# Kernel tuning notes

Hardware: AMD Instinct MI355X
Metric: run time of the kernel (lower is better)

## Reference

```python
import jax, jax.numpy as jnp
import numpy as np

NUM_FEATURES = 8
HIDDEN_DIM = 256
NUM_STABILIZERS = 2048
B, S = 128, 2048


def setup_inputs() -> dict:
    key = jax.random.key(0)
    ks = jax.random.split(key, 8)
    x = jax.random.normal(ks[0], (B, S, NUM_FEATURES), dtype=jnp.float32)
    final_mask = jax.random.randint(ks[1], (B, S), 0, 3, dtype=jnp.int64)
    # stacked per-feature Linear(1, hidden): W[f, h] = weight of proj f, b[f, h] = bias
    xav = float(np.sqrt(6.0 / (1 + HIDDEN_DIM)))  # xavier_uniform for Linear(1, H)
    W = jax.random.uniform(ks[2], (NUM_FEATURES, HIDDEN_DIM), minval=-xav, maxval=xav, dtype=jnp.float32)
    b = jnp.zeros((NUM_FEATURES, HIDDEN_DIM), dtype=jnp.float32)
    index_embed = 0.02 * jax.random.normal(ks[3], (NUM_STABILIZERS, HIDDEN_DIM), dtype=jnp.float32)
    final_on = jax.random.normal(ks[4], (HIDDEN_DIM,), dtype=jnp.float32)
    final_off = jax.random.normal(ks[5], (HIDDEN_DIM,), dtype=jnp.float32)
    gamma = jnp.ones((HIDDEN_DIM,), dtype=jnp.float32)
    beta = jnp.zeros((HIDDEN_DIM,), dtype=jnp.float32)
    return {"x": x, "final_mask": final_mask, "W": W, "b": b,
            "index_embed": index_embed, "final_on": final_on,
            "final_off": final_off, "gamma": gamma, "beta": beta}


def reference(x, final_mask, W, b, index_embed, final_on, final_off, gamma, beta):
    Bx, Sx, _ = x.shape
    # sum of per-feature Linear(1,H): single GEMM + summed bias
    h = jnp.einsum('bsf,fh->bsh', x, W) + b.sum(axis=0)  # [B,S,H]
    h = h + index_embed[:Sx][None, :, :]
    h = h + (final_mask == 1)[..., None] * final_on
    h = h + (final_mask == 2)[..., None] * final_off
    # LayerNorm over last dim, eps=1e-5 (torch default)
    mu = h.mean(axis=-1, keepdims=True)
    var = h.var(axis=-1, keepdims=True)
    h = (h - mu) * jax.lax.rsqrt(var + 1e-5)
    return h * gamma + beta
```

## Files before the change

kernel.cpp:

```cpp
#include <hip/hip_runtime.h>

#define HID 256
#define NFEAT 8
#define SLEN 2048

__global__ __launch_bounds__(256) void p0_base_kernel(
    const float* __restrict__ bias,
    const float* __restrict__ ie,
    float* __restrict__ base2,
    int total4)
{
    const int idx = blockIdx.x * blockDim.x + threadIdx.x;
    if (idx >= total4) return;
    const int h0 = (idx & (HID / 4 - 1)) << 2;
    float4 r = *reinterpret_cast<const float4*>(ie + (size_t)idx * 4);
#pragma unroll
    for (int f = 0; f < NFEAT; ++f) {
        const float4 b4 = *reinterpret_cast<const float4*>(bias + f * HID + h0);
        r.x += b4.x; r.y += b4.y; r.z += b4.z; r.w += b4.w;
    }
    *reinterpret_cast<float4*>(base2 + (size_t)idx * 4) = r;
}

__global__ __launch_bounds__(256, 4) void a_stats_kernel(
    const float* __restrict__ x,
    const int*   __restrict__ mask,
    const float* __restrict__ W,
    const float* __restrict__ base2,
    const float* __restrict__ fon,
    const float* __restrict__ foff,
    float2* __restrict__ musig,
    int Bdim, int ntokens)
{
    const int lane  = threadIdx.x & 63;
    const int gwave = (blockIdx.x * blockDim.x + threadIdx.x) >> 6;
    const int s     = gwave >> 1;
    const int b     = ((gwave & 1) << 6) + lane;
    if (b >= Bdim) return;
    const int t = b * SLEN + s;

    const float4 x0 = *reinterpret_cast<const float4*>(x + (size_t)t * NFEAT);
    const float4 x1 = *reinterpret_cast<const float4*>(x + (size_t)t * NFEAT + 4);
    const float xs[NFEAT] = {x0.x, x0.y, x0.z, x0.w, x1.x, x1.y, x1.z, x1.w};
    const int m = mask[t];
    const float fm1 = (m == 1) ? 1.0f : 0.0f;
    const float fm2 = (m == 2) ? 1.0f : 0.0f;

    float s1 = 0.0f, s2 = 0.0f;
    for (int h0 = 0; h0 < HID; h0 += 4) {
        float4 acc = *reinterpret_cast<const float4*>(base2 + s * HID + h0);
#pragma unroll
        for (int f = 0; f < NFEAT; ++f) {
            const float4 w4 = *reinterpret_cast<const float4*>(W + f * HID + h0);
            acc.x = fmaf(xs[f], w4.x, acc.x);
            acc.y = fmaf(xs[f], w4.y, acc.y);
            acc.z = fmaf(xs[f], w4.z, acc.z);
            acc.w = fmaf(xs[f], w4.w, acc.w);
        }
        const float4 on4 = *reinterpret_cast<const float4*>(fon  + h0);
        const float4 of4 = *reinterpret_cast<const float4*>(foff + h0);
        acc.x += fm1 * on4.x + fm2 * of4.x;
        acc.y += fm1 * on4.y + fm2 * of4.y;
        acc.z += fm1 * on4.z + fm2 * of4.z;
        acc.w += fm1 * on4.w + fm2 * of4.w;
        s1 += acc.x + acc.y + acc.z + acc.w;
        s2 = fmaf(acc.x, acc.x, s2);
        s2 = fmaf(acc.y, acc.y, s2);
        s2 = fmaf(acc.z, acc.z, s2);
        s2 = fmaf(acc.w, acc.w, s2);
    }
    const float mu   = s1 * (1.0f / HID);
    const float var  = s2 * (1.0f / HID) - mu * mu;
    const float rstd = rsqrtf(var + 1e-5f);
    musig[t] = make_float2(mu, rstd);
}

__global__ __launch_bounds__(256, 4) void b_apply_kernel(
    const float* __restrict__ x,
    const int*   __restrict__ mask,
    const float* __restrict__ W,
    const float* __restrict__ base2,
    const float* __restrict__ fon,
    const float* __restrict__ foff,
    const float* __restrict__ gamma,
    const float* __restrict__ beta,
    const float2* __restrict__ musig,
    float* __restrict__ out,
    int ntokens)
{
    const int lane = threadIdx.x & 63;
    const int wavesPerBlock = blockDim.x >> 6;
    const int gwave = blockIdx.x * wavesPerBlock + (threadIdx.x >> 6);
    const int nwaves = gridDim.x * wavesPerBlock;
    const int h0 = lane << 2;

    float wc[NFEAT][4];
#pragma unroll
    for (int f = 0; f < NFEAT; ++f) {
        const float4 w4 = *reinterpret_cast<const float4*>(W + f * HID + h0);
        wc[f][0] = w4.x; wc[f][1] = w4.y; wc[f][2] = w4.z; wc[f][3] = w4.w;
    }
    const float4 g4  = *reinterpret_cast<const float4*>(gamma + h0);
    const float4 be4 = *reinterpret_cast<const float4*>(beta  + h0);

    for (int t = gwave; t < ntokens; t += nwaves) {
        const int s = t & (SLEN - 1);

        const float2 ms = musig[t];
        float4 acc = *reinterpret_cast<const float4*>(base2 + (size_t)s * HID + h0);
        const float4 x0 = *reinterpret_cast<const float4*>(x + (size_t)t * NFEAT);
        const float4 x1 = *reinterpret_cast<const float4*>(x + (size_t)t * NFEAT + 4);
        const int m = mask[t];

        if (m == 1) {
            const float4 on4 = *reinterpret_cast<const float4*>(fon + h0);
            acc.x += on4.x; acc.y += on4.y; acc.z += on4.z; acc.w += on4.w;
        } else if (m == 2) {
            const float4 of4 = *reinterpret_cast<const float4*>(foff + h0);
            acc.x += of4.x; acc.y += of4.y; acc.z += of4.z; acc.w += of4.w;
        }

        const float xs[NFEAT] = {x0.x, x0.y, x0.z, x0.w, x1.x, x1.y, x1.z, x1.w};
#pragma unroll
        for (int f = 0; f < NFEAT; ++f) {
            acc.x = fmaf(xs[f], wc[f][0], acc.x);
            acc.y = fmaf(xs[f], wc[f][1], acc.y);
            acc.z = fmaf(xs[f], wc[f][2], acc.z);
            acc.w = fmaf(xs[f], wc[f][3], acc.w);
        }

        float4 o4;
        o4.x = (acc.x - ms.x) * ms.y * g4.x + be4.x;
        o4.y = (acc.y - ms.x) * ms.y * g4.y + be4.y;
        o4.z = (acc.z - ms.x) * ms.y * g4.z + be4.z;
        o4.w = (acc.w - ms.x) * ms.y * g4.w + be4.w;
        *reinterpret_cast<float4*>(out + (size_t)t * HID + h0) = o4;
    }
}

extern "C" void kernel_launch(void* const* d_in, const int* in_sizes, int n_in,
                              void* d_out, int out_size, void* d_ws, size_t ws_size,
                              hipStream_t stream) {
    const float* x     = (const float*)d_in[0];
    const int*   mask  = (const int*)  d_in[1];
    const float* W     = (const float*)d_in[2];
    const float* bias  = (const float*)d_in[3];
    const float* ie    = (const float*)d_in[4];
    const float* fon   = (const float*)d_in[5];
    const float* foff  = (const float*)d_in[6];
    const float* gamma = (const float*)d_in[7];
    const float* beta  = (const float*)d_in[8];
    float* out = (float*)d_out;

    const int ntokens = in_sizes[0] / NFEAT;
    const int Bdim    = ntokens / SLEN;

    float*  base2 = (float*)d_ws;
    float2* musig = (float2*)((char*)d_ws + (size_t)SLEN * HID * sizeof(float));

    {
        const int total4 = SLEN * HID / 4;
        p0_base_kernel<<<(total4 + 255) / 256, 256, 0, stream>>>(bias, ie, base2, total4);
    }
    {
        const int waves = 2 * SLEN;
        a_stats_kernel<<<(waves * 64) / 256, 256, 0, stream>>>(
            x, mask, W, base2, fon, foff, musig, Bdim, ntokens);
    }
    {
        b_apply_kernel<<<2048, 256, 0, stream>>>(
            x, mask, W, base2, fon, foff, gamma, beta, musig, out, ntokens);
    }
}
```

Measured before the change: 327.7 us.

## Compute LayerNorm stats algebraically from precomputed Gram tables instead of per-hidden loop

Row mean and variance are now computed in closed form: a build kernel precomputes per-position dot products of the base vector with W, on and off, plus a W Gram matrix and related constants. The stats kernel then evaluates a small quadratic form over the 8 features, replacing the 256-wide loop it ran per token. The apply kernel also hoists the on/off loads, unrolls its token loop by two, and writes output with nontemporal stores. The expanded variance formula can lose precision through cancellation.

```diff
diff --git a/kernel.cpp b/kernel.cpp
--- a/kernel.cpp
+++ b/kernel.cpp
@@ -4,38 +4,100 @@
 #define NFEAT 8
 #define SLEN 2048
 
-__global__ __launch_bounds__(256) void p0_base_kernel(
-    const float* __restrict__ bias,
-    const float* __restrict__ ie,
-    float* __restrict__ base2,
-    int total4)
+typedef float v4f __attribute__((ext_vector_type(4)));
+
+__device__ __forceinline__ float wave_sum(float v) {
+#pragma unroll
+    for (int o = 32; o > 0; o >>= 1) v += __shfl_xor(v, o, 64);
+    return v;
+}
+
+__global__ __launch_bounds__(64) void k1_build(
+    const float* __restrict__ bias, const float* __restrict__ ie,
+    const float* __restrict__ W,    const float* __restrict__ fon,
+    const float* __restrict__ foff,
+    float* __restrict__ base2, float* __restrict__ tab, float* __restrict__ cst)
 {
-    const int idx = blockIdx.x * blockDim.x + threadIdx.x;
-    if (idx >= total4) return;
-    const int h0 = (idx & (HID / 4 - 1)) << 2;
-    float4 r = *reinterpret_cast<const float4*>(ie + (size_t)idx * 4);
+    const int lane = threadIdx.x;
+    const int h0 = lane << 2;
+
+    float wc[NFEAT][4];
 #pragma unroll
     for (int f = 0; f < NFEAT; ++f) {
-        const float4 b4 = *reinterpret_cast<const float4*>(bias + f * HID + h0);
-        r.x += b4.x; r.y += b4.y; r.z += b4.z; r.w += b4.w;
-    }
-    *reinterpret_cast<float4*>(base2 + (size_t)idx * 4) = r;
-}
-
-__global__ __launch_bounds__(256, 4) void a_stats_kernel(
-    const float* __restrict__ x,
-    const int*   __restrict__ mask,
-    const float* __restrict__ W,
-    const float* __restrict__ base2,
-    const float* __restrict__ fon,
-    const float* __restrict__ foff,
-    float2* __restrict__ musig,
-    int Bdim, int ntokens)
+        const float4 w4 = *reinterpret_cast<const float4*>(W + f * HID + h0);
+        wc[f][0] = w4.x; wc[f][1] = w4.y; wc[f][2] = w4.z; wc[f][3] = w4.w;
+    }
+    const float4 on4 = *reinterpret_cast<const float4*>(fon  + h0);
+    const float4 of4 = *reinterpret_cast<const float4*>(foff + h0);
+    const float on[4]  = {on4.x, on4.y, on4.z, on4.w};
+    const float off[4] = {of4.x, of4.y, of4.z, of4.w};
+
+    if (blockIdx.x < SLEN) {
+        const int s = blockIdx.x;
+        const float4 e4 = *reinterpret_cast<const float4*>(ie + (size_t)s * HID + h0);
+        float b0[4] = {e4.x, e4.y, e4.z, e4.w};
+#pragma unroll
+        for (int f = 0; f < NFEAT; ++f) {
+            const float4 b4 = *reinterpret_cast<const float4*>(bias + f * HID + h0);
+            b0[0] += b4.x; b0[1] += b4.y; b0[2] += b4.z; b0[3] += b4.w;
+        }
+        float r[12];
+        r[0] = b0[0] + b0[1] + b0[2] + b0[3];
+        r[1] = b0[0]*b0[0] + b0[1]*b0[1] + b0[2]*b0[2] + b0[3]*b0[3];
+        r[2] = b0[0]*on[0] + b0[1]*on[1] + b0[2]*on[2] + b0[3]*on[3];
+        r[3] = b0[0]*off[0]+ b0[1]*off[1]+ b0[2]*off[2]+ b0[3]*off[3];
+#pragma unroll
+        for (int f = 0; f < NFEAT; ++f)
+            r[4+f] = b0[0]*wc[f][0] + b0[1]*wc[f][1] + b0[2]*wc[f][2] + b0[3]*wc[f][3];
+#pragma unroll
+        for (int i = 0; i < 12; ++i) r[i] = wave_sum(r[i]);
+
+        float4 b04 = make_float4(b0[0], b0[1], b0[2], b0[3]);
+        *reinterpret_cast<float4*>(base2 + (size_t)s * HID + h0) = b04;
+        if (lane == 0) {
+#pragma unroll
+            for (int i = 0; i < 12; ++i) tab[s * 16 + i] = r[i];
+        }
+    } else {
+        float r[92];
+#pragma unroll
+        for (int f = 0; f < NFEAT; ++f)
+#pragma unroll
+            for (int g = 0; g < NFEAT; ++g)
+                r[f*8+g] = wc[f][0]*wc[g][0] + wc[f][1]*wc[g][1]
+                         + wc[f][2]*wc[g][2] + wc[f][3]*wc[g][3];
+#pragma unroll
+        for (int f = 0; f < NFEAT; ++f)
+            r[64+f] = wc[f][0] + wc[f][1] + wc[f][2] + wc[f][3];
+#pragma unroll
+        for (int f = 0; f < NFEAT; ++f)
+            r[72+f] = on[0]*wc[f][0] + on[1]*wc[f][1] + on[2]*wc[f][2] + on[3]*wc[f][3];
+#pragma unroll
+        for (int f = 0; f < NFEAT; ++f)
+            r[80+f] = off[0]*wc[f][0] + off[1]*wc[f][1] + off[2]*wc[f][2] + off[3]*wc[f][3];
+        r[88] = on[0] + on[1] + on[2] + on[3];
+        r[89] = off[0]+ off[1]+ off[2]+ off[3];
+        r[90] = on[0]*on[0] + on[1]*on[1] + on[2]*on[2] + on[3]*on[3];
+        r[91] = off[0]*off[0]+ off[1]*off[1]+ off[2]*off[2]+ off[3]*off[3];
+#pragma unroll
+        for (int i = 0; i < 92; ++i) r[i] = wave_sum(r[i]);
+        if (lane == 0) {
+#pragma unroll
+            for (int i = 0; i < 92; ++i) cst[i] = r[i];
+        }
+    }
+}
+
+__global__ __launch_bounds__(256, 4) void k2_stats(
+    const float* __restrict__ x, const int* __restrict__ mask,
+    const float* __restrict__ tab, const float* __restrict__ cst,
+    float2* __restrict__ musig, int Bdim)
 {
-    const int lane  = threadIdx.x & 63;
-    const int gwave = (blockIdx.x * blockDim.x + threadIdx.x) >> 6;
-    const int s     = gwave >> 1;
-    const int b     = ((gwave & 1) << 6) + lane;
+    const int tid   = blockIdx.x * blockDim.x + threadIdx.x;
+    const int lane  = tid & 63;
+    const int gwave = tid >> 6;
+    const int b     = gwave >> 5;
+    const int s     = ((gwave & 31) << 6) + lane;
     if (b >= Bdim) return;
     const int t = b * SLEN + s;
 
@@ -46,47 +108,54 @@
     const float fm1 = (m == 1) ? 1.0f : 0.0f;
     const float fm2 = (m == 2) ? 1.0f : 0.0f;
 
-    float s1 = 0.0f, s2 = 0.0f;
-    for (int h0 = 0; h0 < HID; h0 += 4) {
-        float4 acc = *reinterpret_cast<const float4*>(base2 + s * HID + h0);
-#pragma unroll
-        for (int f = 0; f < NFEAT; ++f) {
-            const float4 w4 = *reinterpret_cast<const float4*>(W + f * HID + h0);
-            acc.x = fmaf(xs[f], w4.x, acc.x);
-            acc.y = fmaf(xs[f], w4.y, acc.y);
-            acc.z = fmaf(xs[f], w4.z, acc.z);
-            acc.w = fmaf(xs[f], w4.w, acc.w);
-        }
-        const float4 on4 = *reinterpret_cast<const float4*>(fon  + h0);
-        const float4 of4 = *reinterpret_cast<const float4*>(foff + h0);
-        acc.x += fm1 * on4.x + fm2 * of4.x;
-        acc.y += fm1 * on4.y + fm2 * of4.y;
-        acc.z += fm1 * on4.z + fm2 * of4.z;
-        acc.w += fm1 * on4.w + fm2 * of4.w;
-        s1 += acc.x + acc.y + acc.z + acc.w;
-        s2 = fmaf(acc.x, acc.x, s2);
-        s2 = fmaf(acc.y, acc.y, s2);
-        s2 = fmaf(acc.z, acc.z, s2);
-        s2 = fmaf(acc.w, acc.w, s2);
-    }
+    const float4* tab4 = reinterpret_cast<const float4*>(tab + (size_t)s * 16);
+    const float4 t0 = tab4[0];
+    const float4 q0 = tab4[1];
+    const float4 q1 = tab4[2];
+    float qf[NFEAT] = {q0.x, q0.y, q0.z, q0.w, q1.x, q1.y, q1.z, q1.w};
+
+    const float4* c4 = reinterpret_cast<const float4*>(cst);
+    const float4 sw0 = c4[16], sw1 = c4[17];
+    const float4 so0 = c4[18], so1 = c4[19];
+    const float4 sf0 = c4[20], sf1 = c4[21];
+    const float4 sc  = c4[22];
+    const float sw[NFEAT]   = {sw0.x, sw0.y, sw0.z, sw0.w, sw1.x, sw1.y, sw1.z, sw1.w};
+    const float sonw[NFEAT] = {so0.x, so0.y, so0.z, so0.w, so1.x, so1.y, so1.z, so1.w};
+    const float sofw[NFEAT] = {sf0.x, sf0.y, sf0.z, sf0.w, sf1.x, sf1.y, sf1.z, sf1.w};
+
+#pragma unroll
+    for (int f = 0; f < NFEAT; ++f)
+        qf[f] += fm1 * sonw[f] + fm2 * sofw[f];
+
+    float s1 = t0.x + fm1 * sc.x + fm2 * sc.y;
+#pragma unroll
+    for (int f = 0; f < NFEAT; ++f) s1 = fmaf(xs[f], sw[f], s1);
+
+    float s2 = t0.y + fm1 * (2.0f * t0.z + sc.z) + fm2 * (2.0f * t0.w + sc.w);
+#pragma unroll
+    for (int f = 0; f < NFEAT; ++f) {
+        const float4 wa = c4[f * 2];
+        const float4 wb = c4[f * 2 + 1];
+        float tf = 2.0f * qf[f];
+        tf = fmaf(wa.x, xs[0], tf); tf = fmaf(wa.y, xs[1], tf);
+        tf = fmaf(wa.z, xs[2], tf); tf = fmaf(wa.w, xs[3], tf);
+        tf = fmaf(wb.x, xs[4], tf); tf = fmaf(wb.y, xs[5], tf);
+        tf = fmaf(wb.z, xs[6], tf); tf = fmaf(wb.w, xs[7], tf);
+        s2 = fmaf(xs[f], tf, s2);
+    }
+
     const float mu   = s1 * (1.0f / HID);
     const float var  = s2 * (1.0f / HID) - mu * mu;
     const float rstd = rsqrtf(var + 1e-5f);
     musig[t] = make_float2(mu, rstd);
 }
 
-__global__ __launch_bounds__(256, 4) void b_apply_kernel(
-    const float* __restrict__ x,
-    const int*   __restrict__ mask,
-    const float* __restrict__ W,
-    const float* __restrict__ base2,
-    const float* __restrict__ fon,
-    const float* __restrict__ foff,
-    const float* __restrict__ gamma,
-    const float* __restrict__ beta,
-    const float2* __restrict__ musig,
-    float* __restrict__ out,
-    int ntokens)
+__global__ __launch_bounds__(256, 4) void k3_apply(
+    const float* __restrict__ x, const int* __restrict__ mask,
+    const float* __restrict__ W, const float* __restrict__ base2,
+    const float* __restrict__ fon, const float* __restrict__ foff,
+    const float* __restrict__ gamma, const float* __restrict__ beta,
+    const float2* __restrict__ musig, float* __restrict__ out, int ntokens)
 {
     const int lane = threadIdx.x & 63;
     const int wavesPerBlock = blockDim.x >> 6;
@@ -102,24 +171,21 @@
     }
     const float4 g4  = *reinterpret_cast<const float4*>(gamma + h0);
     const float4 be4 = *reinterpret_cast<const float4*>(beta  + h0);
-
-    for (int t = gwave; t < ntokens; t += nwaves) {
+    const float4 on4 = *reinterpret_cast<const float4*>(fon   + h0);
+    const float4 of4 = *reinterpret_cast<const float4*>(foff  + h0);
+
+    auto process = [&](int t) {
         const int s = t & (SLEN - 1);
-
         const float2 ms = musig[t];
         float4 acc = *reinterpret_cast<const float4*>(base2 + (size_t)s * HID + h0);
         const float4 x0 = *reinterpret_cast<const float4*>(x + (size_t)t * NFEAT);
         const float4 x1 = *reinterpret_cast<const float4*>(x + (size_t)t * NFEAT + 4);
         const int m = mask[t];
-
         if (m == 1) {
-            const float4 on4 = *reinterpret_cast<const float4*>(fon + h0);
             acc.x += on4.x; acc.y += on4.y; acc.z += on4.z; acc.w += on4.w;
         } else if (m == 2) {
-            const float4 of4 = *reinterpret_cast<const float4*>(foff + h0);
             acc.x += of4.x; acc.y += of4.y; acc.z += of4.z; acc.w += of4.w;
         }
-
         const float xs[NFEAT] = {x0.x, x0.y, x0.z, x0.w, x1.x, x1.y, x1.z, x1.w};
 #pragma unroll
         for (int f = 0; f < NFEAT; ++f) {
@@ -128,14 +194,20 @@
             acc.z = fmaf(xs[f], wc[f][2], acc.z);
             acc.w = fmaf(xs[f], wc[f][3], acc.w);
         }
-
-        float4 o4;
-        o4.x = (acc.x - ms.x) * ms.y * g4.x + be4.x;
-        o4.y = (acc.y - ms.x) * ms.y * g4.y + be4.y;
-        o4.z = (acc.z - ms.x) * ms.y * g4.z + be4.z;
-        o4.w = (acc.w - ms.x) * ms.y * g4.w + be4.w;
-        *reinterpret_cast<float4*>(out + (size_t)t * HID + h0) = o4;
-    }
+        v4f o;
+        o.x = (acc.x - ms.x) * ms.y * g4.x + be4.x;
+        o.y = (acc.y - ms.x) * ms.y * g4.y + be4.y;
+        o.z = (acc.z - ms.x) * ms.y * g4.z + be4.z;
+        o.w = (acc.w - ms.x) * ms.y * g4.w + be4.w;
+        __builtin_nontemporal_store(o, reinterpret_cast<v4f*>(out + (size_t)t * HID + h0));
+    };
+
+    int t = gwave;
+    for (; t + nwaves < ntokens; t += 2 * nwaves) {
+        process(t);
+        process(t + nwaves);
+    }
+    if (t < ntokens) process(t);
 }
 
 extern "C" void kernel_launch(void* const* d_in, const int* in_sizes, int n_in,
@@ -155,20 +227,19 @@
     const int ntokens = in_sizes[0] / NFEAT;
     const int Bdim    = ntokens / SLEN;
 
-    float*  base2 = (float*)d_ws;
-    float2* musig = (float2*)((char*)d_ws + (size_t)SLEN * HID * sizeof(float));
+    char* ws = (char*)d_ws;
+    float*  base2 = (float*)(ws);
+    float*  tab   = (float*)(ws + (1u << 21));
+    float*  cst   = (float*)(ws + (1u << 21) + (1u << 18));
+    float2* musig = (float2*)(ws + (1u << 21) + (1u << 18) + (1u << 16));
+
+    k1_build<<<SLEN + 1, 64, 0, stream>>>(bias, ie, W, fon, foff, base2, tab, cst);
 
     {
-        const int total4 = SLEN * HID / 4;
-        p0_base_kernel<<<(total4 + 255) / 256, 256, 0, stream>>>(bias, ie, base2, total4);
-    }
-    {
-        const int waves = 2 * SLEN;
-        a_stats_kernel<<<(waves * 64) / 256, 256, 0, stream>>>(
-            x, mask, W, base2, fon, foff, musig, Bdim, ntokens);
-    }
-    {
-        b_apply_kernel<<<2048, 256, 0, stream>>>(
-            x, mask, W, base2, fon, foff, gamma, beta, musig, out, ntokens);
-    }
-}
+        const int blocks = (Bdim * 32 * 64) / 256;
+        k2_stats<<<blocks, 256, 0, stream>>>(x, mask, tab, cst, musig, Bdim);
+    }
+
+    k3_apply<<<2048, 256, 0, stream>>>(
+        x, mask, W, base2, fon, foff, gamma, beta, musig, out, ntokens);
+}
```

New measurement: 341.1 us. +4.1%, slower.
